# Kernel optimization log

Hardware: AMD Instinct MI355X
Metric: run time of the kernel (lower is better)

## Reference

```python
import jax, jax.numpy as jnp
import numpy as np

K_FUTURE = 3
GAMMA = 0.25
LAMBDA_CP = 0.1
EPS = 1e-08


def setup_inputs() -> dict:
    key = jax.random.key(0)
    ks = jax.random.split(key, 8)
    B, T, d, Kc = 64, 512, 1024, 256
    Z = jax.random.normal(ks[0], (B, T, d), dtype=jnp.float32)
    # torch init: uniform(-1/Kc, 1/Kc)
    codebook = jax.random.uniform(ks[1], (Kc, d), dtype=jnp.float32,
                                  minval=-1.0 / Kc, maxval=1.0 / Kc)
    s = 1.0 / np.sqrt(d)
    gru_Wih = jax.random.normal(ks[2], (3 * d, d), dtype=jnp.float32) * s
    gru_Whh = jax.random.normal(ks[3], (3 * d, d), dtype=jnp.float32) * s
    gru_bih = jnp.zeros((3 * d,), jnp.float32)
    gru_bhh = jnp.zeros((3 * d,), jnp.float32)
    proj_W = jax.random.normal(ks[4], (d, d), dtype=jnp.float32) * s
    proj_b = jnp.zeros((d,), jnp.float32)
    return {"Z": Z, "codebook": codebook, "gru_Wih": gru_Wih, "gru_Whh": gru_Whh,
            "gru_bih": gru_bih, "gru_bhh": gru_bhh, "proj_W": proj_W, "proj_b": proj_b}


def _gru(x, Wih, Whh, bih, bhh):
    # x: (B, T, d) -> hidden states (B, T, d); torch GRU gate math
    B, T, d = x.shape

    def step(h, xt):
        gi = xt @ Wih.T + bih
        gh = h @ Whh.T + bhh
        i_r, i_z, i_n = jnp.split(gi, 3, axis=-1)
        h_r, h_z, h_n = jnp.split(gh, 3, axis=-1)
        r = jax.nn.sigmoid(i_r + h_r)
        z = jax.nn.sigmoid(i_z + h_z)
        n = jnp.tanh(i_n + r * h_n)
        h_new = (1.0 - z) * n + z * h
        return h_new, h_new

    h0 = jnp.zeros((B, d), x.dtype)
    _, hs = jax.lax.scan(step, h0, jnp.swapaxes(x, 0, 1))
    return jnp.swapaxes(hs, 0, 1)


def _quantize(Z, codebook):
    B, T, d = Z.shape
    flat = Z.reshape(-1, d)                                   # (N, d)
    # squared euclidean distances; argmin identical to cdist(p=2)
    d2 = (jnp.sum(flat * flat, axis=1, keepdims=True)
          - 2.0 * flat @ codebook.T
          + jnp.sum(codebook * codebook, axis=1)[None, :])    # (N, Kc)
    idx = jnp.argmin(d2, axis=1)                              # (N,)
    quantized = codebook[idx].reshape(B, T, d)
    return quantized, idx.reshape(B, T)


def _context_loss(Z, quantized, gru_Wih, gru_Whh, gru_bih, gru_bhh, proj_W, proj_b):
    B, T, d = Z.shape
    hs = _gru(quantized, gru_Wih, gru_Whh, gru_bih, gru_bhh)
    h = hs @ proj_W.T + proj_b                                # (B, T, d)
    total = jnp.float32(0.0)
    for k in range(1, K_FUTURE + 1):
        if T <= k:
            continue
        hk = h[:, :T - k]                                     # (B, T-k, d)
        zk = Z[:, k:]                                         # (B, T-k, d)
        pos = jnp.einsum('btd,btd->bt', hk, zk)               # (B, T-k)
        # sum over tau of mean over batch
        pos_loss = jnp.sum(jnp.mean(-jnp.log(jax.nn.sigmoid(pos) + EPS), axis=0))
        # negatives use a random batch permutation; the mean over (b, c) is
        # permutation-invariant, so compute the full pairwise logits.
        neg = jnp.einsum('btd,ctd->tbc', hk, zk)              # (T-k, B, B)
        neg_loss = jnp.sum(jnp.mean(-jnp.log(1.0 - jax.nn.sigmoid(neg) + EPS), axis=(1, 2)))
        total = total + pos_loss + LAMBDA_CP * neg_loss
    if K_FUTURE > 0 and T > K_FUTURE:
        total = total / (K_FUTURE * (T - K_FUTURE))
    return total


def _vq_loss(Z, quantized):
    commitment = jnp.mean((jax.lax.stop_gradient(Z) - quantized) ** 2)
    codebook_l = jnp.mean((Z - jax.lax.stop_gradient(quantized)) ** 2)
    return commitment + GAMMA * codebook_l


def reference(Z, codebook, gru_Wih, gru_Whh, gru_bih, gru_bhh, proj_W, proj_b):
    quantized, indices = _quantize(Z, codebook)
    L_cp = _context_loss(Z, quantized, gru_Wih, gru_Whh, gru_bih, gru_bhh, proj_W, proj_b)
    L_vq = _vq_loss(Z, quantized)
    L_total = L_cp + L_vq
    return quantized, indices, L_total, L_cp, L_vq
```

## Files before the change

kernel.cpp:

```cpp
#include <hip/hip_runtime.h>
#include <hip/hip_bf16.h>

#define B_ 64
#define T_ 512
#define D_ 1024
#define NQ_ (B_*T_*D_)
#define NI_ (B_*T_)

typedef __attribute__((ext_vector_type(8))) short bf16x8;
typedef __attribute__((ext_vector_type(4))) float f32x4;

__device__ inline ushort f2bf(float f) {
    uint x = __float_as_uint(f);
    return (ushort)((x + 0x7FFFu + ((x >> 16) & 1u)) >> 16);
}
__device__ inline float bf2f(ushort u) { return __uint_as_float(((uint)u) << 16); }

__device__ __forceinline__ void astore(ushort* p, ushort v) {
    __hip_atomic_store(p, v, __ATOMIC_RELAXED, __HIP_MEMORY_SCOPE_AGENT);
}

typedef const __attribute__((address_space(1))) void GV;
typedef __attribute__((address_space(3))) void LV;
__device__ __forceinline__ void gll16(const void* g, void* l) {
    __builtin_amdgcn_global_load_lds((GV*)g, (LV*)l, 16, 0, 0);
}

__device__ __forceinline__ float sigf(float x) { return 1.0f / (1.0f + __expf(-x)); }
__device__ __forceinline__ float tanhfast(float x) {
    float e = __expf(-2.0f * fabsf(x));
    float t = (1.0f - e) / (1.0f + e);
    return copysignf(t, x);
}

__global__ __launch_bounds__(256) void conv_kernel(const float* __restrict__ src,
                                                   ushort* __restrict__ dst, int n) {
    int i = (blockIdx.x * 256 + threadIdx.x) * 4;
    if (i >= n) return;
    float4 v = *reinterpret_cast<const float4*>(src + i);
    ushort4 o;
    o.x = f2bf(v.x); o.y = f2bf(v.y); o.z = f2bf(v.z); o.w = f2bf(v.w);
    *reinterpret_cast<ushort4*>(dst + i) = o;
}

__global__ __launch_bounds__(256) void whhfr_kernel(const float* __restrict__ Whh,
                                                    ushort* __restrict__ Whh_fr) {
    int l = threadIdx.x & 63;
    int unit = blockIdx.x * 4 + (threadIdx.x >> 6);
    int c = unit & 31;
    int g = (unit >> 5) % 3;
    int jb = unit / 96;
    int row = g * 1024 + jb * 16 + (l & 15);
    int k0 = c * 32 + (l >> 4) * 8;
    const float* s = Whh + (size_t)row * 1024 + k0;
    float4 f0 = *reinterpret_cast<const float4*>(s);
    float4 f1 = *reinterpret_cast<const float4*>(s + 4);
    uint4 pk;
    pk.x = (uint)f2bf(f0.x) | ((uint)f2bf(f0.y) << 16);
    pk.y = (uint)f2bf(f0.z) | ((uint)f2bf(f0.w) << 16);
    pk.z = (uint)f2bf(f1.x) | ((uint)f2bf(f1.y) << 16);
    pk.w = (uint)f2bf(f1.z) | ((uint)f2bf(f1.w) << 16);
    reinterpret_cast<uint4*>(Whh_fr)[(size_t)unit * 64 + l] = pk;
}

__device__ inline float np_pairwise_sq_1024(const float* a) {
    float L[8];
    for (int c = 0; c < 8; ++c) {
        const float* p = a + c * 128;
        float r[8];
        #pragma unroll
        for (int k = 0; k < 8; ++k) r[k] = __fmul_rn(p[k], p[k]);
        for (int i = 8; i < 128; i += 8) {
            #pragma unroll
            for (int k = 0; k < 8; ++k) {
                float v = p[i + k];
                r[k] = __fadd_rn(r[k], __fmul_rn(v, v));
            }
        }
        L[c] = __fadd_rn(__fadd_rn(__fadd_rn(r[0], r[1]), __fadd_rn(r[2], r[3])),
                         __fadd_rn(__fadd_rn(r[4], r[5]), __fadd_rn(r[6], r[7])));
    }
    return __fadd_rn(__fadd_rn(__fadd_rn(L[0], L[1]), __fadd_rn(L[2], L[3])),
                     __fadd_rn(__fadd_rn(L[4], L[5]), __fadd_rn(L[6], L[7])));
}

__global__ __launch_bounds__(256) void c2_kernel(const float* __restrict__ cb,
                                                 float* __restrict__ c2) {
    int j = threadIdx.x;
    c2[j] = np_pairwise_sq_1024(cb + (size_t)j * D_);
}

__global__ __launch_bounds__(256) void quantize_kernel(const float* __restrict__ Z,
                                                       const float* __restrict__ cb,
                                                       const float* __restrict__ c2,
                                                       float* __restrict__ qout,
                                                       float* __restrict__ idxout,
                                                       int* __restrict__ idxT,
                                                       double* __restrict__ vq_sum) {
    __shared__ float rows[8][D_];
    __shared__ float z2s[8];
    __shared__ float d2s[256];
    __shared__ int   idxs[256];
    __shared__ int   bestIdx[8];
    __shared__ double redv[256];
    int tid = threadIdx.x;
    size_t row0 = (size_t)blockIdx.x * 8;

    for (int p = 0; p < 8; ++p) {
        float4 v = *reinterpret_cast<const float4*>(Z + (row0 + p) * D_ + tid * 4);
        *reinterpret_cast<float4*>(&rows[p][tid * 4]) = v;
    }
    __syncthreads();

    if (tid < 8) z2s[tid] = np_pairwise_sq_1024(rows[tid]);

    float g2[8];
    #pragma unroll
    for (int r = 0; r < 8; ++r) g2[r] = 0.0f;
    const float* crow = cb + (size_t)tid * D_;
    for (int e = 0; e < D_; e += 4) {
        float4 cv = *reinterpret_cast<const float4*>(crow + e);
        #pragma unroll
        for (int r = 0; r < 8; ++r) {
            g2[r] = __fmaf_rn(__fmul_rn(2.0f, rows[r][e]),     cv.x, g2[r]);
            g2[r] = __fmaf_rn(__fmul_rn(2.0f, rows[r][e + 1]), cv.y, g2[r]);
            g2[r] = __fmaf_rn(__fmul_rn(2.0f, rows[r][e + 2]), cv.z, g2[r]);
            g2[r] = __fmaf_rn(__fmul_rn(2.0f, rows[r][e + 3]), cv.w, g2[r]);
        }
    }
    __syncthreads();

    for (int r = 0; r < 8; ++r) {
        d2s[tid] = __fadd_rn(__fsub_rn(z2s[r], g2[r]), c2[tid]);
        idxs[tid] = tid;
        __syncthreads();
        for (int s = 128; s > 0; s >>= 1) {
            if (tid < s) {
                float ov = d2s[tid + s]; int oi = idxs[tid + s];
                if (ov < d2s[tid] || (ov == d2s[tid] && oi < idxs[tid])) {
                    d2s[tid] = ov; idxs[tid] = oi;
                }
            }
            __syncthreads();
        }
        if (tid == 0) bestIdx[r] = idxs[0];
        __syncthreads();
    }

    if (tid < 8) {
        int row = (int)row0 + tid;
        idxout[row] = (float)bestIdx[tid];
        idxT[((row & 511) << 6) + (row >> 9)] = bestIdx[tid];
    }

    double vqp = 0.0;
    for (int r = 0; r < 8; ++r) {
        int bi = bestIdx[r];
        float4 v = *reinterpret_cast<const float4*>(cb + (size_t)bi * D_ + tid * 4);
        *reinterpret_cast<float4*>(qout + (row0 + r) * D_ + tid * 4) = v;
        const float* zr = &rows[r][tid * 4];
        double d0 = (double)zr[0] - (double)v.x;
        double d1 = (double)zr[1] - (double)v.y;
        double d2 = (double)zr[2] - (double)v.z;
        double d3 = (double)zr[3] - (double)v.w;
        vqp += d0*d0 + d1*d1 + d2*d2 + d3*d3;
    }
    redv[tid] = vqp; __syncthreads();
    for (int s = 128; s > 0; s >>= 1) {
        if (tid < s) redv[tid] += redv[tid + s];
        __syncthreads();
    }
    if (tid == 0) atomicAdd(vq_sum, redv[0]);
}

__global__ __launch_bounds__(256) void gmat_kernel(const float* __restrict__ cb,
                                                   const float* __restrict__ Wih,
                                                   const float* __restrict__ bih,
                                                   const float* __restrict__ bhh,
                                                   ushort* __restrict__ Gp) {
    int m0 = blockIdx.x * 64;
    int n0 = blockIdx.y * 64;
    __shared__ ushort As[64][136];
    __shared__ ushort Bs[64][136];
    int tid = threadIdx.x;
    int w = tid >> 6, l = tid & 63, lr = l & 15, lk = l >> 4;
    f32x4 acc[4];
    #pragma unroll
    for (int i = 0; i < 4; ++i) acc[i] = f32x4{0.f, 0.f, 0.f, 0.f};

    for (int kc = 0; kc < D_; kc += 128) {
        for (int v = tid; v < 2048; v += 256) {
            int r = (v >> 4) & 63, kp = (v & 15) << 3;
            const float* src = (v < 1024) ? (cb  + (size_t)(m0 + r) * D_ + kc + kp)
                                          : (Wih + (size_t)(n0 + r) * D_ + kc + kp);
            float4 f0 = *reinterpret_cast<const float4*>(src);
            float4 f1 = *reinterpret_cast<const float4*>(src + 4);
            uint4 pk;
            pk.x = (uint)f2bf(f0.x) | ((uint)f2bf(f0.y) << 16);
            pk.y = (uint)f2bf(f0.z) | ((uint)f2bf(f0.w) << 16);
            pk.z = (uint)f2bf(f1.x) | ((uint)f2bf(f1.y) << 16);
            pk.w = (uint)f2bf(f1.z) | ((uint)f2bf(f1.w) << 16);
            ushort* dst = (v < 1024) ? &As[r][kp] : &Bs[r][kp];
            *reinterpret_cast<uint4*>(dst) = pk;
        }
        __syncthreads();
        #pragma unroll
        for (int kk = 0; kk < 4; ++kk) {
            bf16x8 bb = *reinterpret_cast<const bf16x8*>(&Bs[(w << 4) + lr][(kk << 5) + (lk << 3)]);
            #pragma unroll
            for (int mi = 0; mi < 4; ++mi) {
                bf16x8 a = *reinterpret_cast<const bf16x8*>(&As[(mi << 4) + lr][(kk << 5) + (lk << 3)]);
                acc[mi] = __builtin_amdgcn_mfma_f32_16x16x32_bf16(a, bb, acc[mi], 0, 0, 0);
            }
        }
        __syncthreads();
    }
    int n = n0 + (w << 4) + lr;
    int gate = n >> 10, jj = n & 1023;
    float bias = bih[n] + (gate < 2 ? bhh[n] : 0.0f);
    #pragma unroll
    for (int mi = 0; mi < 4; ++mi)
        #pragma unroll
        for (int reg = 0; reg < 4; ++reg) {
            int m = m0 + (mi << 4) + (lk << 2) + reg;
            Gp[((((size_t)m << 10) | jj) << 2) + gate] = f2bf(acc[mi][reg] + bias);
        }
}

__global__ __launch_bounds__(256, 1) void recur_kernel(
    const ushort* __restrict__ Whh_fr,
    const ushort* __restrict__ Gp,
    const int*    __restrict__ idxT,
    const float*  __restrict__ bhh,
    ushort* h_hist,
    uint*   flags)
{
    extern __shared__ ushort dynlds[];
    const int tid = threadIdx.x, blk = blockIdx.x;
    const int w = tid >> 6, l = tid & 63;
    const int lr = l & 15, lk = l >> 4;
    const int j0 = blk << 4, j = j0 + lr;
    const int b_base = (w << 4) + (lk << 2);
    const float bhhn = bhh[2048 + j];
    const ushort* Bbase = Whh_fr + (size_t)blk * 49152;
    ushort* myfrag = dynlds + (w << 14);
    const int rowoff = (((w << 4) + lr) << 10) + (lk << 3);
    float hfp[4] = {0.f, 0.f, 0.f, 0.f};
    bool dead = false;

    for (int t = 0; t < T_; ++t) {
        const ushort* src = h_hist + ((size_t)(t == 0 ? 512 : t - 1) << 16) + rowoff;
        #pragma unroll
        for (int c = 0; c < 32; ++c)
            gll16(src + (c << 5), myfrag + (c << 9));
        __syncthreads();

        f32x4 acc0 = {0.f,0.f,0.f,0.f}, acc1 = acc0, acc2 = acc0;
        #pragma unroll
        for (int c = 0; c < 32; ++c) {
            bf16x8 a = *reinterpret_cast<const bf16x8*>(myfrag + (c << 9) + (l << 3));
            bf16x8 b0 = *reinterpret_cast<const bf16x8*>(Bbase +         (c << 9) + (l << 3));
            bf16x8 b1 = *reinterpret_cast<const bf16x8*>(Bbase + 16384 + (c << 9) + (l << 3));
            bf16x8 b2 = *reinterpret_cast<const bf16x8*>(Bbase + 32768 + (c << 9) + (l << 3));
            acc0 = __builtin_amdgcn_mfma_f32_16x16x32_bf16(a, b0, acc0, 0, 0, 0);
            acc1 = __builtin_amdgcn_mfma_f32_16x16x32_bf16(a, b1, acc1, 0, 0, 0);
            acc2 = __builtin_amdgcn_mfma_f32_16x16x32_bf16(a, b2, acc2, 0, 0, 0);
        }

        ushort* hw = h_hist + ((size_t)t << 16);
        const uint4 it4 = *reinterpret_cast<const uint4*>(idxT + (t << 6) + b_base);
        const int* itp = (const int*)&it4;
        #pragma unroll
        for (int reg = 0; reg < 4; ++reg) {
            const int b = b_base + reg;
            const ushort4 g4 = *reinterpret_cast<const ushort4*>(Gp + ((((size_t)itp[reg] << 10) | j) << 2));
            float rr = sigf(bf2f(g4.x) + acc0[reg]);
            float zz = sigf(bf2f(g4.y) + acc1[reg]);
            float nn = tanhfast(bf2f(g4.z) + rr * (acc2[reg] + bhhn));
            float hn = (1.0f - zz) * nn + zz * hfp[reg];
            hfp[reg] = hn;
            astore(&hw[(b << 10) + j], f2bf(hn));
        }

        if (t < T_ - 1) {
            __syncthreads();
            if (tid == 0)
                __hip_atomic_store(&flags[blk << 4], (uint)(t + 1),
                                   __ATOMIC_RELAXED, __HIP_MEMORY_SCOPE_AGENT);
            if (!dead) {
                uint spins = 0;
                while (__hip_atomic_load(&flags[(tid & 63) << 4], __ATOMIC_RELAXED,
                                         __HIP_MEMORY_SCOPE_AGENT) < (uint)(t + 1)) {
                    if (++spins > (1u << 20)) { dead = true; break; }
                }
            }
            __syncthreads();
        }
    }
}

__global__ __launch_bounds__(256) void proj_gemm_kernel(const ushort* __restrict__ h_hist,
                                                        const ushort* __restrict__ projW_bf,
                                                        const float* __restrict__ projb,
                                                        ushort* __restrict__ hproj,
                                                        int ch) {
    int t = ch * 256 + blockIdx.x;
    int n0 = blockIdx.y * 64;
    __shared__ ushort As[64][136];
    __shared__ ushort Bs[64][136];
    int tid = threadIdx.x;
    int w = tid >> 6, l = tid & 63, lr = l & 15, lk = l >> 4;
    f32x4 acc[4];
    #pragma unroll
    for (int i = 0; i < 4; ++i) acc[i] = f32x4{0.f,0.f,0.f,0.f};

    for (int kc = 0; kc < D_; kc += 128) {
        for (int v = tid; v < 2048; v += 256) {
            int r = (v >> 4) & 63, kp = (v & 15) << 3;
            if (v < 1024)
                *reinterpret_cast<uint4*>(&As[r][kp]) =
                    *reinterpret_cast<const uint4*>(h_hist + ((size_t)t << 16) + ((size_t)r << 10) + kc + kp);
            else
                *reinterpret_cast<uint4*>(&Bs[r][kp]) =
                    *reinterpret_cast<const uint4*>(projW_bf + ((size_t)(n0 + r) << 10) + kc + kp);
        }
        __syncthreads();
        #pragma unroll
        for (int kk = 0; kk < 4; ++kk) {
            bf16x8 bb = *reinterpret_cast<const bf16x8*>(&Bs[(w << 4) + lr][(kk << 5) + (lk << 3)]);
            #pragma unroll
            for (int mi = 0; mi < 4; ++mi) {
                bf16x8 a = *reinterpret_cast<const bf16x8*>(&As[(mi << 4) + lr][(kk << 5) + (lk << 3)]);
                acc[mi] = __builtin_amdgcn_mfma_f32_16x16x32_bf16(a, bb, acc[mi], 0, 0, 0);
            }
        }
        __syncthreads();
    }
    int n = n0 + (w << 4) + lr;
    float pb = projb[n];
    #pragma unroll
    for (int mi = 0; mi < 4; ++mi)
        #pragma unroll
        for (int reg = 0; reg < 4; ++reg) {
            int b = (mi << 4) + (lk << 2) + reg;
            hproj[((size_t)(t & 255) << 16) + (b << 10) + n] = f2bf(acc[mi][reg] + pb);
        }
}

__global__ __launch_bounds__(256) void cpc_loss_kernel(const ushort* __restrict__ hproj,
                                                       const float* __restrict__ Z,
                                                       double* __restrict__ cp_sum,
                                                       int ch) {
    int tp = ch * 256 + blockIdx.x;
    int k = blockIdx.y + 1;
    if (tp >= T_ - k) return;
    __shared__ float Hs[64][33];
    __shared__ float Zs[64][33];
    int tid = threadIdx.x;
    int tx = tid & 15, ty = tid >> 4;
    float acc[4][4] = {};
    const ushort* Hbase = hproj + ((size_t)(tp & 255) << 16);
    const float* Zbase = Z + (size_t)(tp + k) * D_;
    const size_t zstride = (size_t)T_ * D_;
    int r = tid >> 3, c = (tid & 7) << 2;

    for (int kc = 0; kc < D_; kc += 32) {
        #pragma unroll
        for (int p = 0; p < 2; ++p) {
            int rr2 = r + 32 * p;
            ushort4 hv = *reinterpret_cast<const ushort4*>(Hbase + (size_t)rr2 * D_ + kc + c);
            float4 zv = *reinterpret_cast<const float4*>(Zbase + (size_t)rr2 * zstride + kc + c);
            Hs[rr2][c] = bf2f(hv.x); Hs[rr2][c+1] = bf2f(hv.y);
            Hs[rr2][c+2] = bf2f(hv.z); Hs[rr2][c+3] = bf2f(hv.w);
            Zs[rr2][c] = zv.x; Zs[rr2][c+1] = zv.y; Zs[rr2][c+2] = zv.z; Zs[rr2][c+3] = zv.w;
        }
        __syncthreads();
        #pragma unroll
        for (int kk = 0; kk < 32; ++kk) {
            float av[4], bv[4];
            #pragma unroll
            for (int i = 0; i < 4; ++i) av[i] = Hs[ty + 16*i][kk];
            #pragma unroll
            for (int jv = 0; jv < 4; ++jv) bv[jv] = Zs[tx + 16*jv][kk];
            #pragma unroll
            for (int i = 0; i < 4; ++i)
                #pragma unroll
                for (int jv = 0; jv < 4; ++jv)
                    acc[i][jv] = __fmaf_rn(av[i], bv[jv], acc[i][jv]);
        }
        __syncthreads();
    }

    double lsum = 0.0;
    #pragma unroll
    for (int i = 0; i < 4; ++i) {
        #pragma unroll
        for (int jv = 0; jv < 4; ++jv) {
            int bb = ty + 16*i, cc2 = tx + 16*jv;
            double v = (double)acc[i][jv];
            double sg = 1.0 / (1.0 + exp(-v));
            lsum += (0.1 / 4096.0) * (-log(1.0 - sg + 1e-8));
            if (bb == cc2) lsum += (1.0 / 64.0) * (-log(sg + 1e-8));
        }
    }
    __shared__ double red[256];
    red[tid] = lsum; __syncthreads();
    for (int s2 = 128; s2 > 0; s2 >>= 1) {
        if (tid < s2) red[tid] += red[tid + s2];
        __syncthreads();
    }
    if (tid == 0) atomicAdd(cp_sum, red[0]);
}

__global__ void finalize_kernel(const double* __restrict__ accum,
                                float* __restrict__ scal) {
    double cp = accum[0] / 1527.0;
    double vq = accum[1] * 1.25 / (double)NQ_;
    scal[0] = (float)(cp + vq);
    scal[1] = (float)cp;
    scal[2] = (float)vq;
}

extern "C" void kernel_launch(void* const* d_in, const int* in_sizes, int n_in,
                              void* d_out, int out_size, void* d_ws, size_t ws_size,
                              hipStream_t stream) {
    const float* Z     = (const float*)d_in[0];
    const float* cb    = (const float*)d_in[1];
    const float* Wih   = (const float*)d_in[2];
    const float* Whh   = (const float*)d_in[3];
    const float* bih   = (const float*)d_in[4];
    const float* bhh   = (const float*)d_in[5];
    const float* projW = (const float*)d_in[6];
    const float* projb = (const float*)d_in[7];

    float* out       = (float*)d_out;
    float* quantized = out;
    float* idxout    = out + (size_t)NQ_;
    float* scal      = out + (size_t)NQ_ + NI_;

    char* p = (char*)d_ws;
    ushort* Whh_fr   = (ushort*)p;  p += 6291456;
    ushort* projW_bf = (ushort*)p;  p += 2097152;
    ushort* Gp       = (ushort*)p;  p += 2097152;
    int*    idxT     = (int*)p;     p += 131072;
    float*  c2f      = (float*)p;   p += 4096;
    char*   ctrl     = p;           p += 8192;
    ushort* h_hist   = (ushort*)p;  p += (size_t)513 * 131072;
    ushort* hproj    = (ushort*)p;  p += (size_t)256 * 131072;

    uint*   flags = (uint*)ctrl;
    double* accum = (double*)(ctrl + 4096);

    hipMemsetAsync(ctrl, 0, 8192, stream);
    hipMemsetAsync(h_hist + ((size_t)512 << 16), 0, 131072, stream);

    conv_kernel<<<1024, 256, 0, stream>>>(projW, projW_bf, 1048576);
    whhfr_kernel<<<1536, 256, 0, stream>>>(Whh, Whh_fr);
    c2_kernel<<<1, 256, 0, stream>>>(cb, c2f);
    quantize_kernel<<<4096, 256, 0, stream>>>(Z, cb, c2f, quantized, idxout, idxT,
                                              &accum[1]);
    gmat_kernel<<<dim3(4, 48), 256, 0, stream>>>(cb, Wih, bih, bhh, Gp);

    hipFuncSetAttribute(reinterpret_cast<const void*>(recur_kernel),
                        hipFuncAttributeMaxDynamicSharedMemorySize, 131072);
    recur_kernel<<<dim3(64), dim3(256), 131072, stream>>>(Whh_fr, Gp, idxT, bhh,
                                                          h_hist, flags);

    for (int ch = 0; ch < 2; ++ch) {
        proj_gemm_kernel<<<dim3(256, 16), 256, 0, stream>>>(h_hist, projW_bf, projb, hproj, ch);
        cpc_loss_kernel<<<dim3(256, 3), 256, 0, stream>>>(hproj, Z, &accum[0], ch);
    }

    finalize_kernel<<<1, 1, 0, stream>>>(accum, scal);
}
```

Baseline: 5.912 ms.

## Fuse projection GEMM and CPC loss into one per-timestep tail kernel

Replaces the chunked projection GEMM plus CPC-loss kernels with a single per-timestep kernel. Each block stages the whole h_t tile in LDS, computes the projection tile by tile with MFMA, and immediately feeds each 64-column slice into bf16 MFMA dot products against Z at t+1..t+3. The fused kernel removes the hproj round trip through global memory and the FP32 scalar loss GEMM. projW is pre-packed into a fragment-ordered layout. In exchange the Z operand of the loss logits is now rounded to bf16, and the kernel runs one 140KB-LDS block per CU over 512 blocks.

```diff
diff --git a/kernel.cpp b/kernel.cpp
--- a/kernel.cpp
+++ b/kernel.cpp
@@ -31,16 +31,6 @@
     float e = __expf(-2.0f * fabsf(x));
     float t = (1.0f - e) / (1.0f + e);
     return copysignf(t, x);
-}
-
-__global__ __launch_bounds__(256) void conv_kernel(const float* __restrict__ src,
-                                                   ushort* __restrict__ dst, int n) {
-    int i = (blockIdx.x * 256 + threadIdx.x) * 4;
-    if (i >= n) return;
-    float4 v = *reinterpret_cast<const float4*>(src + i);
-    ushort4 o;
-    o.x = f2bf(v.x); o.y = f2bf(v.y); o.z = f2bf(v.z); o.w = f2bf(v.w);
-    *reinterpret_cast<ushort4*>(dst + i) = o;
 }
 
 __global__ __launch_bounds__(256) void whhfr_kernel(const float* __restrict__ Whh,
@@ -61,6 +51,25 @@
     pk.z = (uint)f2bf(f1.x) | ((uint)f2bf(f1.y) << 16);
     pk.w = (uint)f2bf(f1.z) | ((uint)f2bf(f1.w) << 16);
     reinterpret_cast<uint4*>(Whh_fr)[(size_t)unit * 64 + l] = pk;
+}
+
+__global__ __launch_bounds__(256) void pwfr_kernel(const float* __restrict__ projW,
+                                                   ushort* __restrict__ pW_fr) {
+    int l = threadIdx.x & 63;
+    int unit = blockIdx.x * 4 + (threadIdx.x >> 6);
+    int c = unit & 31;
+    int ng = unit >> 5;
+    int row = ng * 16 + (l & 15);
+    int k0 = c * 32 + (l >> 4) * 8;
+    const float* s = projW + (size_t)row * 1024 + k0;
+    float4 f0 = *reinterpret_cast<const float4*>(s);
+    float4 f1 = *reinterpret_cast<const float4*>(s + 4);
+    uint4 pk;
+    pk.x = (uint)f2bf(f0.x) | ((uint)f2bf(f0.y) << 16);
+    pk.y = (uint)f2bf(f0.z) | ((uint)f2bf(f0.w) << 16);
+    pk.z = (uint)f2bf(f1.x) | ((uint)f2bf(f1.y) << 16);
+    pk.w = (uint)f2bf(f1.z) | ((uint)f2bf(f1.w) << 16);
+    reinterpret_cast<uint4*>(pW_fr)[(size_t)unit * 64 + l] = pk;
 }
 
 __device__ inline float np_pairwise_sq_1024(const float* a) {
@@ -299,117 +308,107 @@
     }
 }
 
-__global__ __launch_bounds__(256) void proj_gemm_kernel(const ushort* __restrict__ h_hist,
-                                                        const ushort* __restrict__ projW_bf,
-                                                        const float* __restrict__ projb,
-                                                        ushort* __restrict__ hproj,
-                                                        int ch) {
-    int t = ch * 256 + blockIdx.x;
-    int n0 = blockIdx.y * 64;
-    __shared__ ushort As[64][136];
-    __shared__ ushort Bs[64][136];
-    int tid = threadIdx.x;
-    int w = tid >> 6, l = tid & 63, lr = l & 15, lk = l >> 4;
-    f32x4 acc[4];
+__global__ __launch_bounds__(256, 1) void tail_kernel(
+    const ushort* __restrict__ h_hist,
+    const ushort* __restrict__ pW_fr,
+    const float*  __restrict__ projb,
+    const float*  __restrict__ Z,
+    double* __restrict__ cp_sum)
+{
+    extern __shared__ ushort dynlds[];
+    ushort* hp = dynlds + 65536;
+    const int t = blockIdx.x;
+    const int tid = threadIdx.x;
+    const int w = tid >> 6, l = tid & 63;
+    const int lr = l & 15, lk = l >> 4;
+
+    const ushort* hsrc = h_hist + ((size_t)t << 16);
     #pragma unroll
-    for (int i = 0; i < 4; ++i) acc[i] = f32x4{0.f,0.f,0.f,0.f};
-
-    for (int kc = 0; kc < D_; kc += 128) {
-        for (int v = tid; v < 2048; v += 256) {
-            int r = (v >> 4) & 63, kp = (v & 15) << 3;
-            if (v < 1024)
-                *reinterpret_cast<uint4*>(&As[r][kp]) =
-                    *reinterpret_cast<const uint4*>(h_hist + ((size_t)t << 16) + ((size_t)r << 10) + kc + kp);
-            else
-                *reinterpret_cast<uint4*>(&Bs[r][kp]) =
-                    *reinterpret_cast<const uint4*>(projW_bf + ((size_t)(n0 + r) << 10) + kc + kp);
-        }
-        __syncthreads();
-        #pragma unroll
-        for (int kk = 0; kk < 4; ++kk) {
-            bf16x8 bb = *reinterpret_cast<const bf16x8*>(&Bs[(w << 4) + lr][(kk << 5) + (lk << 3)]);
+    for (int i = 0; i < 32; ++i) {
+        int u = (w << 5) + i;
+        int c = u >> 2, mi = u & 3;
+        const ushort* s = hsrc + ((size_t)((mi << 4) + lr) << 10) + (c << 5) + (lk << 3);
+        gll16(s, dynlds + (u << 9));
+    }
+    __syncthreads();
+
+    const int kfmax = (t < T_ - 3) ? 3 : (t < T_ - 2 ? 2 : (t < T_ - 1 ? 1 : 0));
+    f32x4 accg[3][4];
+    #pragma unroll
+    for (int a = 0; a < 3; ++a)
+        #pragma unroll
+        for (int b = 0; b < 4; ++b) accg[a][b] = f32x4{0.f,0.f,0.f,0.f};
+
+    for (int nt = 0; nt < 16; ++nt) {
+        f32x4 accp[4];
+        #pragma unroll
+        for (int i = 0; i < 4; ++i) accp[i] = f32x4{0.f,0.f,0.f,0.f};
+        const ushort* pwb = pW_fr + ((size_t)((nt << 2) + w) << 14);
+        for (int c = 0; c < 32; ++c) {
+            bf16x8 bfr = *reinterpret_cast<const bf16x8*>(pwb + (c << 9) + (l << 3));
             #pragma unroll
             for (int mi = 0; mi < 4; ++mi) {
-                bf16x8 a = *reinterpret_cast<const bf16x8*>(&As[(mi << 4) + lr][(kk << 5) + (lk << 3)]);
-                acc[mi] = __builtin_amdgcn_mfma_f32_16x16x32_bf16(a, bb, acc[mi], 0, 0, 0);
-            }
-        }
-        __syncthreads();
-    }
-    int n = n0 + (w << 4) + lr;
-    float pb = projb[n];
-    #pragma unroll
-    for (int mi = 0; mi < 4; ++mi)
-        #pragma unroll
-        for (int reg = 0; reg < 4; ++reg) {
-            int b = (mi << 4) + (lk << 2) + reg;
-            hproj[((size_t)(t & 255) << 16) + (b << 10) + n] = f2bf(acc[mi][reg] + pb);
-        }
-}
-
-__global__ __launch_bounds__(256) void cpc_loss_kernel(const ushort* __restrict__ hproj,
-                                                       const float* __restrict__ Z,
-                                                       double* __restrict__ cp_sum,
-                                                       int ch) {
-    int tp = ch * 256 + blockIdx.x;
-    int k = blockIdx.y + 1;
-    if (tp >= T_ - k) return;
-    __shared__ float Hs[64][33];
-    __shared__ float Zs[64][33];
-    int tid = threadIdx.x;
-    int tx = tid & 15, ty = tid >> 4;
-    float acc[4][4] = {};
-    const ushort* Hbase = hproj + ((size_t)(tp & 255) << 16);
-    const float* Zbase = Z + (size_t)(tp + k) * D_;
-    const size_t zstride = (size_t)T_ * D_;
-    int r = tid >> 3, c = (tid & 7) << 2;
-
-    for (int kc = 0; kc < D_; kc += 32) {
-        #pragma unroll
-        for (int p = 0; p < 2; ++p) {
-            int rr2 = r + 32 * p;
-            ushort4 hv = *reinterpret_cast<const ushort4*>(Hbase + (size_t)rr2 * D_ + kc + c);
-            float4 zv = *reinterpret_cast<const float4*>(Zbase + (size_t)rr2 * zstride + kc + c);
-            Hs[rr2][c] = bf2f(hv.x); Hs[rr2][c+1] = bf2f(hv.y);
-            Hs[rr2][c+2] = bf2f(hv.z); Hs[rr2][c+3] = bf2f(hv.w);
-            Zs[rr2][c] = zv.x; Zs[rr2][c+1] = zv.y; Zs[rr2][c+2] = zv.z; Zs[rr2][c+3] = zv.w;
-        }
-        __syncthreads();
-        #pragma unroll
-        for (int kk = 0; kk < 32; ++kk) {
-            float av[4], bv[4];
-            #pragma unroll
-            for (int i = 0; i < 4; ++i) av[i] = Hs[ty + 16*i][kk];
-            #pragma unroll
-            for (int jv = 0; jv < 4; ++jv) bv[jv] = Zs[tx + 16*jv][kk];
-            #pragma unroll
-            for (int i = 0; i < 4; ++i)
+                bf16x8 afr = *reinterpret_cast<const bf16x8*>(dynlds + (((c << 2) + mi) << 9) + (l << 3));
+                accp[mi] = __builtin_amdgcn_mfma_f32_16x16x32_bf16(afr, bfr, accp[mi], 0, 0, 0);
+            }
+        }
+        float pb = projb[(nt << 6) + (w << 4) + lr];
+        #pragma unroll
+        for (int mi = 0; mi < 4; ++mi)
+            #pragma unroll
+            for (int reg = 0; reg < 4; ++reg) {
+                int b = (mi << 4) + (lk << 2) + reg;
+                hp[b * 72 + (w << 4) + lr] = f2bf(accp[mi][reg] + pb);
+            }
+        __syncthreads();
+
+        for (int kf = 1; kf <= kfmax; ++kf) {
+            const float* zr = Z + ((((size_t)((w << 4) + lr) << 9) + (t + kf)) << 10) + (nt << 6);
+            #pragma unroll
+            for (int ck2 = 0; ck2 < 2; ++ck2) {
+                const float* zc = zr + (ck2 << 5) + (lk << 3);
+                float4 z0 = *reinterpret_cast<const float4*>(zc);
+                float4 z1 = *reinterpret_cast<const float4*>(zc + 4);
+                uint4 pk;
+                pk.x = (uint)f2bf(z0.x) | ((uint)f2bf(z0.y) << 16);
+                pk.y = (uint)f2bf(z0.z) | ((uint)f2bf(z0.w) << 16);
+                pk.z = (uint)f2bf(z1.x) | ((uint)f2bf(z1.y) << 16);
+                pk.w = (uint)f2bf(z1.z) | ((uint)f2bf(z1.w) << 16);
+                bf16x8 zfr = *reinterpret_cast<bf16x8*>(&pk);
                 #pragma unroll
-                for (int jv = 0; jv < 4; ++jv)
-                    acc[i][jv] = __fmaf_rn(av[i], bv[jv], acc[i][jv]);
+                for (int mi2 = 0; mi2 < 4; ++mi2) {
+                    bf16x8 afr = *reinterpret_cast<const bf16x8*>(
+                        hp + ((mi2 << 4) + lr) * 72 + (ck2 << 5) + (lk << 3));
+                    accg[kf - 1][mi2] = __builtin_amdgcn_mfma_f32_16x16x32_bf16(
+                        afr, zfr, accg[kf - 1][mi2], 0, 0, 0);
+                }
+            }
         }
         __syncthreads();
     }
 
     double lsum = 0.0;
-    #pragma unroll
-    for (int i = 0; i < 4; ++i) {
-        #pragma unroll
-        for (int jv = 0; jv < 4; ++jv) {
-            int bb = ty + 16*i, cc2 = tx + 16*jv;
-            double v = (double)acc[i][jv];
-            double sg = 1.0 / (1.0 + exp(-v));
-            lsum += (0.1 / 4096.0) * (-log(1.0 - sg + 1e-8));
-            if (bb == cc2) lsum += (1.0 / 64.0) * (-log(sg + 1e-8));
-        }
-    }
-    __shared__ double red[256];
+    const int c = (w << 4) + lr;
+    for (int kf = 1; kf <= kfmax; ++kf) {
+        #pragma unroll
+        for (int mi2 = 0; mi2 < 4; ++mi2)
+            #pragma unroll
+            for (int reg = 0; reg < 4; ++reg) {
+                int b = (mi2 << 4) + (lk << 2) + reg;
+                double v = (double)accg[kf - 1][mi2][reg];
+                double sg = 1.0 / (1.0 + exp(-v));
+                lsum += (0.1 / 4096.0) * (-log(1.0 - sg + 1e-8));
+                if (b == c) lsum += (1.0 / 64.0) * (-log(sg + 1e-8));
+            }
+    }
+    __syncthreads();
+    double* red = (double*)dynlds;
     red[tid] = lsum; __syncthreads();
     for (int s2 = 128; s2 > 0; s2 >>= 1) {
         if (tid < s2) red[tid] += red[tid + s2];
         __syncthreads();
     }
-    if (tid == 0) atomicAdd(cp_sum, red[0]);
+    if (tid == 0 && kfmax > 0) atomicAdd(cp_sum, red[0]);
 }
 
 __global__ void finalize_kernel(const double* __restrict__ accum,
@@ -439,14 +438,13 @@
     float* scal      = out + (size_t)NQ_ + NI_;
 
     char* p = (char*)d_ws;
-    ushort* Whh_fr   = (ushort*)p;  p += 6291456;
-    ushort* projW_bf = (ushort*)p;  p += 2097152;
-    ushort* Gp       = (ushort*)p;  p += 2097152;
-    int*    idxT     = (int*)p;     p += 131072;
-    float*  c2f      = (float*)p;   p += 4096;
-    char*   ctrl     = p;           p += 8192;
-    ushort* h_hist   = (ushort*)p;  p += (size_t)513 * 131072;
-    ushort* hproj    = (ushort*)p;  p += (size_t)256 * 131072;
+    ushort* Whh_fr = (ushort*)p;  p += 6291456;
+    ushort* pW_fr  = (ushort*)p;  p += 2097152;
+    ushort* Gp     = (ushort*)p;  p += 2097152;
+    int*    idxT   = (int*)p;     p += 131072;
+    float*  c2f    = (float*)p;   p += 4096;
+    char*   ctrl   = p;           p += 8192;
+    ushort* h_hist = (ushort*)p;  p += (size_t)513 * 131072;
 
     uint*   flags = (uint*)ctrl;
     double* accum = (double*)(ctrl + 4096);
@@ -454,8 +452,8 @@
     hipMemsetAsync(ctrl, 0, 8192, stream);
     hipMemsetAsync(h_hist + ((size_t)512 << 16), 0, 131072, stream);
 
-    conv_kernel<<<1024, 256, 0, stream>>>(projW, projW_bf, 1048576);
     whhfr_kernel<<<1536, 256, 0, stream>>>(Whh, Whh_fr);
+    pwfr_kernel<<<512, 256, 0, stream>>>(projW, pW_fr);
     c2_kernel<<<1, 256, 0, stream>>>(cb, c2f);
     quantize_kernel<<<4096, 256, 0, stream>>>(Z, cb, c2f, quantized, idxout, idxT,
                                               &accum[1]);
@@ -466,10 +464,10 @@
     recur_kernel<<<dim3(64), dim3(256), 131072, stream>>>(Whh_fr, Gp, idxT, bhh,
                                                           h_hist, flags);
 
-    for (int ch = 0; ch < 2; ++ch) {
-        proj_gemm_kernel<<<dim3(256, 16), 256, 0, stream>>>(h_hist, projW_bf, projb, hproj, ch);
-        cpc_loss_kernel<<<dim3(256, 3), 256, 0, stream>>>(hproj, Z, &accum[0], ch);
-    }
+    hipFuncSetAttribute(reinterpret_cast<const void*>(tail_kernel),
+                        hipFuncAttributeMaxDynamicSharedMemorySize, 140288);
+    tail_kernel<<<dim3(512), dim3(256), 140288, stream>>>(h_hist, pW_fr, projb, Z,
+                                                          &accum[0]);
 
     finalize_kernel<<<1, 1, 0, stream>>>(accum, scal);
 }
```

Measured after the change: 5.563 ms. 1.06x faster.
